# Kernel tuning notes

Measured on AMD Instinct MI355X. Metric: run time of the kernel, lower is better.

## Reference

```python
import jax, jax.numpy as jnp
import numpy as np

B, S, D = 2, 2048, 2048
H = 16
I = 8192  # intermediate_size
HD = I // H  # per-head intermediate dim = 512


def setup_inputs() -> dict:
    key = jax.random.key(0)
    ks = jax.random.split(key, 7)
    scale_d = 1.0 / np.sqrt(D)
    scale_i = 1.0 / np.sqrt(I)
    return {
        "x": jax.random.normal(ks[0], (B, S, D), dtype=jnp.float32),
        "adjacency": jax.random.uniform(ks[1], (B, H, S, S), dtype=jnp.float32) * (1.0 / S),
        "Wg": jax.random.normal(ks[2], (D, I), dtype=jnp.float32) * scale_d,
        "Wu": jax.random.normal(ks[3], (D, I), dtype=jnp.float32) * scale_d,
        "Wd": jax.random.normal(ks[4], (I, D), dtype=jnp.float32) * scale_i,
        "eps": jnp.zeros((H,), dtype=jnp.float32),
        "alpha": jnp.ones((H,), dtype=jnp.float32),
    }


def reference(x, adjacency, Wg, Wu, Wd, eps, alpha):
    # gate/up projections + SwiGLU: (B,S,I)
    gate = jnp.einsum("bsd,di->bsi", x, Wg)
    up = jnp.einsum("bsd,di->bsi", x, Wu)
    h_inter = jax.nn.silu(gate) * up
    # split into heads: (B,H,S,HD)
    h_heads = h_inter.reshape(B, S, H, HD).transpose(0, 2, 1, 3)
    # batched per-head GIN: (1+eps_h)*h + alpha_h * A_h @ h, all heads at once
    agg = jnp.einsum("bhst,bhtd->bhsd", adjacency, h_heads)
    e = (1.0 + eps)[None, :, None, None]
    a = alpha[None, :, None, None]
    h_gin = e * h_heads + a * agg
    # recombine heads -> (B,S,I), then down projection
    h_comb = h_gin.transpose(0, 2, 1, 3).reshape(B, S, I)
    return jnp.einsum("bsi,id->bsd", h_comb, Wd)
```

## Files before the change

### kernel.cpp

```cpp
#include <hip/hip_runtime.h>
#include <hip/hip_bf16.h>


typedef __bf16 bf16x8 __attribute__((ext_vector_type(8)));
typedef float f32x4 __attribute__((ext_vector_type(4)));

__device__ __forceinline__ unsigned short f2bf(float f) {
    union { float f; unsigned int u; } x; x.f = f;
    unsigned int r = x.u + 0x7fffu + ((x.u >> 16) & 1u);
    return (unsigned short)(r >> 16);
}
__device__ __forceinline__ float bf2f(unsigned short b) {
    union { unsigned int u; float f; } x; x.u = ((unsigned int)b) << 16;
    return x.f;
}

__device__ __forceinline__ void gload_lds16(const void* g, void* l) {
    __builtin_amdgcn_global_load_lds((const __attribute__((address_space(1))) void*)g,
                                     (__attribute__((address_space(3))) void*)l,
                                     16, 0, 0);
}

__device__ __forceinline__ void stage(unsigned short* lds, const unsigned short* g,
                                      int ld, int wave, int lane) {
    int rsub = lane >> 3;
    int j    = lane & 7;
    int jsw  = (j ^ rsub) << 3;
    const unsigned short* src = g + (size_t)(wave * 32 + rsub) * ld + jsw;
    unsigned short* dst = lds + (wave * 32) * 64;
#pragma unroll
    for (int c = 0; c < 4; ++c) {
        gload_lds16((const void*)(src + (size_t)c * 8 * ld), (void*)(dst + c * 8 * 64));
    }
}
__device__ __forceinline__ bf16x8 frag(const unsigned short* lds, int row, int k) {
    int byte = ((row * 64 + k) * 2) ^ ((row & 7) << 4);
    return *(const bf16x8*)((const char*)lds + byte);
}


__global__ void conv_kernel(const float* __restrict__ in, unsigned short* __restrict__ out) {
    size_t i = ((size_t)blockIdx.x * 256 + threadIdx.x) * 4;
    float4 v = *(const float4*)(in + i);
    ushort4 o; o.x = f2bf(v.x); o.y = f2bf(v.y); o.z = f2bf(v.z); o.w = f2bf(v.w);
    *(ushort4*)(out + i) = o;
}

__global__ void tconv_kernel(const float* __restrict__ in, unsigned short* __restrict__ out,
                             int R, int C) {
    __shared__ float tile[64][65];
    int nbc = C >> 6;
    int bc = blockIdx.x % nbc, br = blockIdx.x / nbc;
    int r0 = br * 64, c0 = bc * 64;
    int t = threadIdx.x;
#pragma unroll
    for (int i = 0; i < 4; ++i) {
        int idx = i * 256 + t;
        int r = idx >> 4, c4 = (idx & 15) * 4;
        float4 v = *(const float4*)(in + (size_t)(r0 + r) * C + c0 + c4);
        tile[r][c4] = v.x; tile[r][c4 + 1] = v.y; tile[r][c4 + 2] = v.z; tile[r][c4 + 3] = v.w;
    }
    __syncthreads();
#pragma unroll
    for (int i = 0; i < 4; ++i) {
        int idx = i * 256 + t;
        int c = idx >> 4, r4 = (idx & 15) * 4;
        ushort4 o;
        o.x = f2bf(tile[r4][c]); o.y = f2bf(tile[r4 + 1][c]);
        o.z = f2bf(tile[r4 + 2][c]); o.w = f2bf(tile[r4 + 3][c]);
        *(ushort4*)(out + (size_t)(c0 + c) * R + r0 + r4) = o;
    }
}

template<int EPI>
__global__ void __launch_bounds__(512, 2) gemm256(
    const unsigned short* __restrict__ Ag,
    const unsigned short* __restrict__ Bg,
    const unsigned short* __restrict__ gbuf_c,
    unsigned short* __restrict__ gbuf,
    unsigned short* __restrict__ hh,
    unsigned short* __restrict__ hhT)
{
    const int K = 2048;
    __shared__ unsigned short LDS[4][16384];
    int bid = (int)blockIdx.x;
    int lb = (bid & 7) * 64 + (bid >> 3);
    int nt = lb & 31, mt = lb >> 5;
    int tid = threadIdx.x, lane = tid & 63, wave = tid >> 6;
    int wm = wave >> 2, wn = wave & 3;
    int l15 = lane & 15, l4 = lane >> 4;

    f32x4 acc[8][4] = {};

    int jl = (lane & 7) ^ (lane >> 3);
    int prow0 = wave * 16 + (lane >> 3);
    int row0 = prow0 + ((jl & 4) << 5);
    int cc = (jl & 3) << 3;
    const unsigned short* srcA0 = Ag + (size_t)(mt * 256 + row0) * K + cc;
    const unsigned short* srcA1 = srcA0 + (size_t)8 * K;
    const unsigned short* srcB0 = Bg + (size_t)(nt * 256 + row0) * K + cc;
    const unsigned short* srcB1 = srcB0 + (size_t)8 * K;

    int cA = l15 * 128 + (((l4 + wm * 4) ^ (l15 & 7)) << 4);
    int cB = ((wn & 1) * 64 + l15) * 128 + (((l4 + ((wn >> 1) << 2)) ^ (l15 & 7)) << 4);

#define STAGE_A(t_) do { char* d_ = (char*)&LDS[(t_) & 3][0] + wave * 2048;              \
        gload_lds16((const void*)(srcA0 + (size_t)(t_) * 32), (void*)d_);                \
        gload_lds16((const void*)(srcA1 + (size_t)(t_) * 32), (void*)(d_ + 1024)); } while (0)
#define STAGE_B(t_) do { char* d_ = (char*)&LDS[(t_) & 3][8192] + wave * 2048;           \
        gload_lds16((const void*)(srcB0 + (size_t)(t_) * 32), (void*)d_);                \
        gload_lds16((const void*)(srcB1 + (size_t)(t_) * 32), (void*)(d_ + 1024)); } while (0)

    STAGE_A(0); STAGE_B(0);
    STAGE_A(1); STAGE_B(1);

    for (int t = 0; t < 64; ++t) {
        asm volatile("s_waitcnt vmcnt(4)" ::: "memory");
        __builtin_amdgcn_s_barrier();
        const char* Abase = (const char*)&LDS[t & 3][0];
        const char* Bbase = Abase + 16384;
        bool more = (t + 2) < 64;
        if (more) STAGE_A(t + 2);
        bf16x8 bf[4], af[4];
#pragma unroll
        for (int ni = 0; ni < 4; ++ni) bf[ni] = *(const bf16x8*)(Bbase + cB + ni * 2048);
#pragma unroll
        for (int mi = 0; mi < 4; ++mi) af[mi] = *(const bf16x8*)(Abase + cA + mi * 2048);
        __builtin_amdgcn_s_setprio(1);
#pragma unroll
        for (int mi = 0; mi < 4; ++mi)
#pragma unroll
            for (int ni = 0; ni < 4; ++ni)
                acc[mi][ni] = __builtin_amdgcn_mfma_f32_16x16x32_bf16(af[mi], bf[ni], acc[mi][ni], 0, 0, 0);
        __builtin_amdgcn_s_setprio(0);
        if (more) STAGE_B(t + 2);
#pragma unroll
        for (int mi = 0; mi < 4; ++mi) af[mi] = *(const bf16x8*)(Abase + cA + 8192 + mi * 2048);
        __builtin_amdgcn_s_setprio(1);
#pragma unroll
        for (int mi = 0; mi < 4; ++mi)
#pragma unroll
            for (int ni = 0; ni < 4; ++ni)
                acc[4 + mi][ni] = __builtin_amdgcn_mfma_f32_16x16x32_bf16(af[mi], bf[ni], acc[4 + mi][ni], 0, 0, 0);
        __builtin_amdgcn_s_setprio(0);
    }
#undef STAGE_A
#undef STAGE_B

    if (EPI == 0) {
        ushort4* g4 = (ushort4*)gbuf;
        size_t base = ((size_t)lb * 32) * 512 + tid;
#pragma unroll
        for (int a = 0; a < 8; ++a)
#pragma unroll
            for (int ni = 0; ni < 4; ++ni) {
                f32x4 v = acc[a][ni];
                ushort4 o;
                o.x = f2bf(v[0]); o.y = f2bf(v[1]); o.z = f2bf(v[2]); o.w = f2bf(v[3]);
                g4[base + (size_t)(a * 4 + ni) * 512] = o;
            }
    } else {
        const ushort4* g4 = (const ushort4*)gbuf_c;
        size_t base = ((size_t)lb * 32) * 512 + tid;
        int rowb = mt * 256 + wm * 128 + l4 * 4;
        int colb = nt * 256 + wn * 64 + l15;
        int b = mt >> 3;
#pragma unroll
        for (int a = 0; a < 8; ++a)
#pragma unroll
            for (int ni = 0; ni < 4; ++ni) {
                ushort4 gq = g4[base + (size_t)(a * 4 + ni) * 512];
                int row = rowb + a * 16;
                int n = colb + ni * 16;
                ushort4 hv;
#pragma unroll
                for (int r = 0; r < 4; ++r) {
                    float gv = bf2f(((const unsigned short*)&gq)[r]);
                    float u = acc[a][ni][r];
                    float h = gv / (1.f + __expf(-gv)) * u;
                    unsigned short hb = f2bf(h);
                    ((unsigned short*)&hv)[r] = hb;
                    hh[(size_t)(row + r) * 8192 + n] = hb;
                }
                *(ushort4*)(hhT + ((size_t)b * 8192 + n) * 2048 + (row & 2047)) = hv;
            }
    }
}

__global__ void __launch_bounds__(512) gemm_agg2(
    const float* __restrict__ adj,
    const unsigned short* __restrict__ hhT,
    const unsigned short* __restrict__ hh,
    const float* __restrict__ eps, const float* __restrict__ alpha,
    unsigned short* __restrict__ hcomb)
{
    const int S = 2048, HD = 512, I = 8192;
    __shared__ unsigned short As[128 * 40];
    __shared__ unsigned short Bs[512 * 40];
    int bid = (int)blockIdx.x;
    int lb = (bid & 7) * 64 + (bid >> 3);
    int pair = lb >> 4;
    int mt = lb & 15;
    int b = pair >> 4, h = pair & 15;
    int tid = threadIdx.x;
    int lane = tid & 63;
    int wave = tid >> 6;
    int wm = wave >> 2, wn = wave & 3;
    f32x4 acc[4][8] = {};

    const float* Ab = adj + ((size_t)pair * S + (size_t)mt * 128) * S;
    const unsigned short* Bb = hhT + ((size_t)b * I + (size_t)h * HD) * (size_t)S;

    float4 pa0, pa1;
    int4 pb0, pb1, pb2, pb3;
    int a_row0 = tid >> 3, a_c = (tid & 7) << 2;
    int b_row0 = tid >> 2, b_ch = (tid & 3) << 3;

#define AGG_LOAD(K0)                                                              \
    do {                                                                          \
        pa0 = *(const float4*)(Ab + (size_t)a_row0 * S + (K0) + a_c);             \
        pa1 = *(const float4*)(Ab + (size_t)(a_row0 + 64) * S + (K0) + a_c);      \
        pb0 = *(const int4*)(Bb + (size_t)b_row0 * S + (K0) + b_ch);              \
        pb1 = *(const int4*)(Bb + (size_t)(b_row0 + 128) * S + (K0) + b_ch);      \
        pb2 = *(const int4*)(Bb + (size_t)(b_row0 + 256) * S + (K0) + b_ch);      \
        pb3 = *(const int4*)(Bb + (size_t)(b_row0 + 384) * S + (K0) + b_ch);      \
    } while (0)

#define AGG_WRITE()                                                               \
    do {                                                                          \
        ushort4 o0, o1;                                                           \
        o0.x = f2bf(pa0.x); o0.y = f2bf(pa0.y); o0.z = f2bf(pa0.z); o0.w = f2bf(pa0.w); \
        o1.x = f2bf(pa1.x); o1.y = f2bf(pa1.y); o1.z = f2bf(pa1.z); o1.w = f2bf(pa1.w); \
        *(ushort4*)((char*)As + a_row0 * 80 + a_c * 2) = o0;                      \
        *(ushort4*)((char*)As + (a_row0 + 64) * 80 + a_c * 2) = o1;               \
        *(int4*)((char*)Bs + b_row0 * 80 + b_ch * 2) = pb0;                       \
        *(int4*)((char*)Bs + (b_row0 + 128) * 80 + b_ch * 2) = pb1;               \
        *(int4*)((char*)Bs + (b_row0 + 256) * 80 + b_ch * 2) = pb2;               \
        *(int4*)((char*)Bs + (b_row0 + 384) * 80 + b_ch * 2) = pb3;               \
    } while (0)

    AGG_LOAD(0);
    AGG_WRITE();
    __syncthreads();

    int lrow = lane & 15;
    int koff2 = ((lane >> 4) << 3) * 2;
    const char* aptr = (const char*)As + (wm * 64 + lrow) * 80 + koff2;
    const char* bptr = (const char*)Bs + (wn * 128 + lrow) * 80 + koff2;

    for (int step = 0; step < 64; ++step) {
        bool more = (step + 1) < 64;
        if (more) AGG_LOAD((step + 1) * 32);
        bf16x8 af[4], bfv[8];
#pragma unroll
        for (int mi = 0; mi < 4; ++mi) af[mi] = *(const bf16x8*)(aptr + mi * 16 * 80);
#pragma unroll
        for (int ni = 0; ni < 8; ++ni) bfv[ni] = *(const bf16x8*)(bptr + ni * 16 * 80);
#pragma unroll
        for (int mi = 0; mi < 4; ++mi)
#pragma unroll
            for (int ni = 0; ni < 8; ++ni)
                acc[mi][ni] = __builtin_amdgcn_mfma_f32_16x16x32_bf16(af[mi], bfv[ni], acc[mi][ni], 0, 0, 0);
        __syncthreads();
        if (more) {
            AGG_WRITE();
            __syncthreads();
        }
    }
#undef AGG_LOAD
#undef AGG_WRITE

    float e1 = 1.f + eps[h];
    float a1 = alpha[h];
    int s_base = mt * 128 + wm * 64;
    int d_base = wn * 128;
#pragma unroll
    for (int mi = 0; mi < 4; ++mi)
#pragma unroll
        for (int ni = 0; ni < 8; ++ni) {
            int sb = s_base + mi * 16 + ((lane >> 4) << 2);
            int d = d_base + ni * 16 + (lane & 15);
#pragma unroll
            for (int r = 0; r < 4; ++r) {
                size_t off = ((size_t)(b * S + sb + r)) * I + (size_t)h * HD + d;
                float hv = bf2f(hh[off]);
                hcomb[off] = f2bf(e1 * hv + a1 * acc[mi][ni][r]);
            }
        }
}

__global__ void __launch_bounds__(256) gemm_out(
    const unsigned short* __restrict__ hcomb,
    const unsigned short* __restrict__ WdT,
    float* __restrict__ out)
{
    const int K = 8192, N = 2048;
    __shared__ unsigned short As[128 * 64], Bs[128 * 64];
    int bid = blockIdx.x;
    int nt = bid & 15, mt = bid >> 4;
    int tid = threadIdx.x, wave = tid >> 6, lane = tid & 63;
    int wm = wave >> 1, wn = wave & 1;
    f32x4 acc[4][4] = {};
    const unsigned short* Ab = hcomb + (size_t)(mt * 128) * K;
    const unsigned short* Bb = WdT + (size_t)(nt * 128) * K;
    for (int k0 = 0; k0 < K; k0 += 64) {
        stage(As, Ab + k0, K, wave, lane);
        stage(Bs, Bb + k0, K, wave, lane);
        __syncthreads();
#pragma unroll
        for (int ki = 0; ki < 2; ++ki) {
            int kk = ki * 32 + ((lane >> 4) << 3);
            bf16x8 af[4], bfv[4];
#pragma unroll
            for (int mi = 0; mi < 4; ++mi) af[mi] = frag(As, wm * 64 + mi * 16 + (lane & 15), kk);
#pragma unroll
            for (int ni = 0; ni < 4; ++ni) bfv[ni] = frag(Bs, wn * 64 + ni * 16 + (lane & 15), kk);
#pragma unroll
            for (int mi = 0; mi < 4; ++mi)
#pragma unroll
                for (int ni = 0; ni < 4; ++ni)
                    acc[mi][ni] = __builtin_amdgcn_mfma_f32_16x16x32_bf16(af[mi], bfv[ni], acc[mi][ni], 0, 0, 0);
        }
        __syncthreads();
    }
    int m_off = mt * 128 + wm * 64, n_off = nt * 128 + wn * 64;
#pragma unroll
    for (int mi = 0; mi < 4; ++mi)
#pragma unroll
        for (int ni = 0; ni < 4; ++ni) {
            int mbase = m_off + mi * 16 + ((lane >> 4) << 2);
            int n = n_off + ni * 16 + (lane & 15);
#pragma unroll
            for (int r = 0; r < 4; ++r)
                out[(size_t)(mbase + r) * N + n] = acc[mi][ni][r];
        }
}

extern "C" void kernel_launch(void* const* d_in, const int* in_sizes, int n_in,
                              void* d_out, int out_size, void* d_ws, size_t ws_size,
                              hipStream_t stream) {
    const float* x     = (const float*)d_in[0];
    const float* adj   = (const float*)d_in[1];
    const float* Wg    = (const float*)d_in[2];
    const float* Wu    = (const float*)d_in[3];
    const float* Wd    = (const float*)d_in[4];
    const float* eps   = (const float*)d_in[5];
    const float* alpha = (const float*)d_in[6];
    float* out = (float*)d_out;

    unsigned short* ws    = (unsigned short*)d_ws;
    unsigned short* xb    = ws;
    unsigned short* WgT   = xb + (size_t)4096 * 2048;
    unsigned short* WuT   = WgT + (size_t)8192 * 2048;
    unsigned short* WdT   = WuT + (size_t)8192 * 2048;
    unsigned short* hh    = WdT + (size_t)2048 * 8192;
    unsigned short* hhT   = hh + (size_t)4096 * 8192;
    unsigned short* hcomb = hhT + (size_t)16384 * 2048;
    unsigned short* gbuf  = hcomb;

    conv_kernel<<<8192, 256, 0, stream>>>(x, xb);
    tconv_kernel<<<4096, 256, 0, stream>>>(Wg, WgT, 2048, 8192);
    tconv_kernel<<<4096, 256, 0, stream>>>(Wu, WuT, 2048, 8192);
    tconv_kernel<<<4096, 256, 0, stream>>>(Wd, WdT, 8192, 2048);
    gemm256<0><<<512, 512, 0, stream>>>(xb, WgT, nullptr, gbuf, nullptr, nullptr);
    gemm256<1><<<512, 512, 0, stream>>>(xb, WuT, gbuf, nullptr, hh, hhT);
    gemm_agg2<<<512, 512, 0, stream>>>(adj, hhT, hh, eps, alpha, hcomb);
    gemm_out<<<32 * 16, 256, 0, stream>>>(hcomb, WdT, out);
}
```

Baseline: 826.9 us.

## Double-buffer aggregation GEMM and pipeline down-projection with async LDS loads

```diff
diff --git a/kernel.cpp b/kernel.cpp
--- a/kernel.cpp
+++ b/kernel.cpp
@@ -19,23 +19,6 @@
     __builtin_amdgcn_global_load_lds((const __attribute__((address_space(1))) void*)g,
                                      (__attribute__((address_space(3))) void*)l,
                                      16, 0, 0);
-}
-
-__device__ __forceinline__ void stage(unsigned short* lds, const unsigned short* g,
-                                      int ld, int wave, int lane) {
-    int rsub = lane >> 3;
-    int j    = lane & 7;
-    int jsw  = (j ^ rsub) << 3;
-    const unsigned short* src = g + (size_t)(wave * 32 + rsub) * ld + jsw;
-    unsigned short* dst = lds + (wave * 32) * 64;
-#pragma unroll
-    for (int c = 0; c < 4; ++c) {
-        gload_lds16((const void*)(src + (size_t)c * 8 * ld), (void*)(dst + c * 8 * 64));
-    }
-}
-__device__ __forceinline__ bf16x8 frag(const unsigned short* lds, int row, int k) {
-    int byte = ((row * 64 + k) * 2) ^ ((row & 7) << 4);
-    return *(const bf16x8*)((const char*)lds + byte);
 }
 
 
@@ -115,7 +98,8 @@
     STAGE_A(1); STAGE_B(1);
 
     for (int t = 0; t < 64; ++t) {
-        asm volatile("s_waitcnt vmcnt(4)" ::: "memory");
+        if (t + 2 < 64) asm volatile("s_waitcnt vmcnt(4)" ::: "memory");
+        else            asm volatile("s_waitcnt vmcnt(0)" ::: "memory");
         __builtin_amdgcn_s_barrier();
         const char* Abase = (const char*)&LDS[t & 3][0];
         const char* Bbase = Abase + 16384;
@@ -187,7 +171,7 @@
     }
 }
 
-__global__ void __launch_bounds__(512) gemm_agg2(
+__global__ void __launch_bounds__(512, 2) gemm_agg3(
     const float* __restrict__ adj,
     const unsigned short* __restrict__ hhT,
     const unsigned short* __restrict__ hh,
@@ -195,8 +179,8 @@
     unsigned short* __restrict__ hcomb)
 {
     const int S = 2048, HD = 512, I = 8192;
-    __shared__ unsigned short As[128 * 40];
-    __shared__ unsigned short Bs[512 * 40];
+    __shared__ unsigned short As[2][128 * 40];
+    __shared__ unsigned short Bs[2][512 * 40];
     int bid = (int)blockIdx.x;
     int lb = (bid & 7) * 64 + (bid >> 3);
     int pair = lb >> 4;
@@ -211,64 +195,84 @@
     const float* Ab = adj + ((size_t)pair * S + (size_t)mt * 128) * S;
     const unsigned short* Bb = hhT + ((size_t)b * I + (size_t)h * HD) * (size_t)S;
 
-    float4 pa0, pa1;
-    int4 pb0, pb1, pb2, pb3;
     int a_row0 = tid >> 3, a_c = (tid & 7) << 2;
     int b_row0 = tid >> 2, b_ch = (tid & 3) << 3;
 
-#define AGG_LOAD(K0)                                                              \
-    do {                                                                          \
-        pa0 = *(const float4*)(Ab + (size_t)a_row0 * S + (K0) + a_c);             \
-        pa1 = *(const float4*)(Ab + (size_t)(a_row0 + 64) * S + (K0) + a_c);      \
-        pb0 = *(const int4*)(Bb + (size_t)b_row0 * S + (K0) + b_ch);              \
-        pb1 = *(const int4*)(Bb + (size_t)(b_row0 + 128) * S + (K0) + b_ch);      \
-        pb2 = *(const int4*)(Bb + (size_t)(b_row0 + 256) * S + (K0) + b_ch);      \
-        pb3 = *(const int4*)(Bb + (size_t)(b_row0 + 384) * S + (K0) + b_ch);      \
+    float4 pa0_0, pa1_0, pa0_1, pa1_1;
+    int4 pb0_0, pb1_0, pb2_0, pb3_0, pb0_1, pb1_1, pb2_1, pb3_1;
+
+#define AGG_LOAD(SET, K0)                                                               \
+    do {                                                                                \
+        pa0_##SET = *(const float4*)(Ab + (size_t)a_row0 * S + (K0) + a_c);             \
+        pa1_##SET = *(const float4*)(Ab + (size_t)(a_row0 + 64) * S + (K0) + a_c);      \
+        pb0_##SET = *(const int4*)(Bb + (size_t)b_row0 * S + (K0) + b_ch);              \
+        pb1_##SET = *(const int4*)(Bb + (size_t)(b_row0 + 128) * S + (K0) + b_ch);      \
+        pb2_##SET = *(const int4*)(Bb + (size_t)(b_row0 + 256) * S + (K0) + b_ch);      \
+        pb3_##SET = *(const int4*)(Bb + (size_t)(b_row0 + 384) * S + (K0) + b_ch);      \
     } while (0)
 
-#define AGG_WRITE()                                                               \
-    do {                                                                          \
-        ushort4 o0, o1;                                                           \
-        o0.x = f2bf(pa0.x); o0.y = f2bf(pa0.y); o0.z = f2bf(pa0.z); o0.w = f2bf(pa0.w); \
-        o1.x = f2bf(pa1.x); o1.y = f2bf(pa1.y); o1.z = f2bf(pa1.z); o1.w = f2bf(pa1.w); \
-        *(ushort4*)((char*)As + a_row0 * 80 + a_c * 2) = o0;                      \
-        *(ushort4*)((char*)As + (a_row0 + 64) * 80 + a_c * 2) = o1;               \
-        *(int4*)((char*)Bs + b_row0 * 80 + b_ch * 2) = pb0;                       \
-        *(int4*)((char*)Bs + (b_row0 + 128) * 80 + b_ch * 2) = pb1;               \
-        *(int4*)((char*)Bs + (b_row0 + 256) * 80 + b_ch * 2) = pb2;               \
-        *(int4*)((char*)Bs + (b_row0 + 384) * 80 + b_ch * 2) = pb3;               \
+#define AGG_WRITE(SET, BUF)                                                             \
+    do {                                                                                \
+        ushort4 o0, o1;                                                                 \
+        o0.x = f2bf(pa0_##SET.x); o0.y = f2bf(pa0_##SET.y);                             \
+        o0.z = f2bf(pa0_##SET.z); o0.w = f2bf(pa0_##SET.w);                             \
+        o1.x = f2bf(pa1_##SET.x); o1.y = f2bf(pa1_##SET.y);                             \
+        o1.z = f2bf(pa1_##SET.z); o1.w = f2bf(pa1_##SET.w);                             \
+        *(ushort4*)((char*)As[BUF] + a_row0 * 80 + a_c * 2) = o0;                       \
+        *(ushort4*)((char*)As[BUF] + (a_row0 + 64) * 80 + a_c * 2) = o1;                \
+        *(int4*)((char*)Bs[BUF] + b_row0 * 80 + b_ch * 2) = pb0_##SET;                  \
+        *(int4*)((char*)Bs[BUF] + (b_row0 + 128) * 80 + b_ch * 2) = pb1_##SET;          \
+        *(int4*)((char*)Bs[BUF] + (b_row0 + 256) * 80 + b_ch * 2) = pb2_##SET;          \
+        *(int4*)((char*)Bs[BUF] + (b_row0 + 384) * 80 + b_ch * 2) = pb3_##SET;          \
     } while (0)
-
-    AGG_LOAD(0);
-    AGG_WRITE();
-    __syncthreads();
 
     int lrow = lane & 15;
     int koff2 = ((lane >> 4) << 3) * 2;
-    const char* aptr = (const char*)As + (wm * 64 + lrow) * 80 + koff2;
-    const char* bptr = (const char*)Bs + (wn * 128 + lrow) * 80 + koff2;
-
-    for (int step = 0; step < 64; ++step) {
-        bool more = (step + 1) < 64;
-        if (more) AGG_LOAD((step + 1) * 32);
-        bf16x8 af[4], bfv[8];
-#pragma unroll
-        for (int mi = 0; mi < 4; ++mi) af[mi] = *(const bf16x8*)(aptr + mi * 16 * 80);
-#pragma unroll
-        for (int ni = 0; ni < 8; ++ni) bfv[ni] = *(const bf16x8*)(bptr + ni * 16 * 80);
-#pragma unroll
-        for (int mi = 0; mi < 4; ++mi)
-#pragma unroll
-            for (int ni = 0; ni < 8; ++ni)
-                acc[mi][ni] = __builtin_amdgcn_mfma_f32_16x16x32_bf16(af[mi], bfv[ni], acc[mi][ni], 0, 0, 0);
-        __syncthreads();
-        if (more) {
-            AGG_WRITE();
-            __syncthreads();
+    const char* aptr0 = (const char*)As[0] + (wm * 64 + lrow) * 80 + koff2;
+    const char* bptr0 = (const char*)Bs[0] + (wn * 128 + lrow) * 80 + koff2;
+    const char* aptr1 = (const char*)As[1] + (wm * 64 + lrow) * 80 + koff2;
+    const char* bptr1 = (const char*)Bs[1] + (wn * 128 + lrow) * 80 + koff2;
+
+#define AGG_COMPUTE(APTR, BPTR)                                                         \
+    do {                                                                                \
+        bf16x8 af[4], bfv[8];                                                           \
+        _Pragma("unroll")                                                               \
+        for (int mi = 0; mi < 4; ++mi) af[mi] = *(const bf16x8*)((APTR) + mi * 16 * 80);\
+        _Pragma("unroll")                                                               \
+        for (int ni = 0; ni < 8; ++ni) bfv[ni] = *(const bf16x8*)((BPTR) + ni * 16 * 80);\
+        __builtin_amdgcn_s_setprio(1);                                                  \
+        _Pragma("unroll")                                                               \
+        for (int mi = 0; mi < 4; ++mi)                                                  \
+            _Pragma("unroll")                                                           \
+            for (int ni = 0; ni < 8; ++ni)                                              \
+                acc[mi][ni] = __builtin_amdgcn_mfma_f32_16x16x32_bf16(af[mi], bfv[ni],  \
+                                                                      acc[mi][ni], 0, 0, 0); \
+        __builtin_amdgcn_s_setprio(0);                                                  \
+    } while (0)
+
+    AGG_LOAD(0, 0);
+    AGG_WRITE(0, 0);
+    AGG_LOAD(1, 32);
+    asm volatile("s_waitcnt lgkmcnt(0)" ::: "memory");
+    __builtin_amdgcn_s_barrier();
+
+    for (int s = 0; s < 64; s += 2) {
+        if (s + 2 < 64) AGG_LOAD(0, (s + 2) * 32);
+        AGG_COMPUTE(aptr0, bptr0);
+        AGG_WRITE(1, 1);
+        asm volatile("s_waitcnt lgkmcnt(0)" ::: "memory");
+        __builtin_amdgcn_s_barrier();
+        if (s + 3 < 64) AGG_LOAD(1, (s + 3) * 32);
+        AGG_COMPUTE(aptr1, bptr1);
+        if (s + 2 < 64) {
+            AGG_WRITE(0, 0);
+            asm volatile("s_waitcnt lgkmcnt(0)" ::: "memory");
+            __builtin_amdgcn_s_barrier();
         }
     }
 #undef AGG_LOAD
 #undef AGG_WRITE
+#undef AGG_COMPUTE
 
     float e1 = 1.f + eps[h];
     float a1 = alpha[h];
@@ -289,50 +293,79 @@
         }
 }
 
-__global__ void __launch_bounds__(256) gemm_out(
+__global__ void __launch_bounds__(512, 2) gemm_out2(
     const unsigned short* __restrict__ hcomb,
     const unsigned short* __restrict__ WdT,
     float* __restrict__ out)
 {
-    const int K = 8192, N = 2048;
-    __shared__ unsigned short As[128 * 64], Bs[128 * 64];
-    int bid = blockIdx.x;
-    int nt = bid & 15, mt = bid >> 4;
-    int tid = threadIdx.x, wave = tid >> 6, lane = tid & 63;
+    const int K = 8192;
+    __shared__ unsigned short LDS[4][12288];
+    int bid = (int)blockIdx.x;
+    int lb = (bid & 7) * 32 + (bid >> 3);
+    int mt = lb >> 4, nt = lb & 15;
+    int tid = threadIdx.x, lane = tid & 63, wave = tid >> 6;
     int wm = wave >> 1, wn = wave & 1;
+    int l15 = lane & 15, l4 = lane >> 4;
     f32x4 acc[4][4] = {};
-    const unsigned short* Ab = hcomb + (size_t)(mt * 128) * K;
-    const unsigned short* Bb = WdT + (size_t)(nt * 128) * K;
-    for (int k0 = 0; k0 < K; k0 += 64) {
-        stage(As, Ab + k0, K, wave, lane);
-        stage(Bs, Bb + k0, K, wave, lane);
-        __syncthreads();
-#pragma unroll
-        for (int ki = 0; ki < 2; ++ki) {
-            int kk = ki * 32 + ((lane >> 4) << 3);
-            bf16x8 af[4], bfv[4];
-#pragma unroll
-            for (int mi = 0; mi < 4; ++mi) af[mi] = frag(As, wm * 64 + mi * 16 + (lane & 15), kk);
-#pragma unroll
-            for (int ni = 0; ni < 4; ++ni) bfv[ni] = frag(Bs, wn * 64 + ni * 16 + (lane & 15), kk);
-#pragma unroll
-            for (int mi = 0; mi < 4; ++mi)
-#pragma unroll
-                for (int ni = 0; ni < 4; ++ni)
-                    acc[mi][ni] = __builtin_amdgcn_mfma_f32_16x16x32_bf16(af[mi], bfv[ni], acc[mi][ni], 0, 0, 0);
-        }
-        __syncthreads();
-    }
-    int m_off = mt * 128 + wm * 64, n_off = nt * 128 + wn * 64;
+
+    int jl = (lane & 7) ^ (lane >> 3);
+    int prowA = wave * 16 + (lane >> 3);
+    int rowA0 = prowA + ((jl & 4) << 5);
+    int ccA = (jl & 3) << 3;
+    const unsigned short* srcA0 = hcomb + (size_t)(mt * 256 + rowA0) * K + ccA;
+    const unsigned short* srcA1 = srcA0 + (size_t)8 * K;
+    int prowB = tid >> 3;
+    int jbl = (tid & 7) ^ (prowB & 7);
+    int rowB0 = prowB + ((jbl & 4) << 4);
+    int ccB = (jbl & 3) << 3;
+    const unsigned short* srcB0 = WdT + (size_t)(nt * 128 + rowB0) * K + ccB;
+
+    int cA0 = ((wm & 1) * 64 + l15) * 128 + (((((wm >> 1) << 2) + l4) ^ (l15 & 7)) << 4);
+    int cB0 = l15 * 128 + ((((wn << 2) + l4) ^ (l15 & 7)) << 4);
+
+#define OSTAGE(t_) do {                                                                  \
+        char* dA = (char*)&LDS[(t_) & 3][0] + wave * 2048;                               \
+        gload_lds16((const void*)(srcA0 + (size_t)(t_) * 32), (void*)dA);                \
+        gload_lds16((const void*)(srcA1 + (size_t)(t_) * 32), (void*)(dA + 1024));       \
+        char* dB = (char*)&LDS[(t_) & 3][8192] + wave * 1024;                            \
+        gload_lds16((const void*)(srcB0 + (size_t)(t_) * 32), (void*)dB);                \
+    } while (0)
+
+    OSTAGE(0); OSTAGE(1);
+
+    for (int t = 0; t < 256; ++t) {
+        if (t + 2 < 256) asm volatile("s_waitcnt vmcnt(3)" ::: "memory");
+        else             asm volatile("s_waitcnt vmcnt(0)" ::: "memory");
+        __builtin_amdgcn_s_barrier();
+        const char* Abase = (const char*)&LDS[t & 3][0];
+        const char* Bbase = Abase + 16384;
+        bool more = (t + 2) < 256;
+        bf16x8 af[4], bf[4];
+#pragma unroll
+        for (int ni = 0; ni < 4; ++ni) bf[ni] = *(const bf16x8*)(Bbase + cB0 + ni * 2048);
+        if (more) OSTAGE(t + 2);
+#pragma unroll
+        for (int mi = 0; mi < 4; ++mi) af[mi] = *(const bf16x8*)(Abase + cA0 + mi * 2048);
+        __builtin_amdgcn_s_setprio(1);
+#pragma unroll
+        for (int mi = 0; mi < 4; ++mi)
+#pragma unroll
+            for (int ni = 0; ni < 4; ++ni)
+                acc[mi][ni] = __builtin_amdgcn_mfma_f32_16x16x32_bf16(af[mi], bf[ni], acc[mi][ni], 0, 0, 0);
+        __builtin_amdgcn_s_setprio(0);
+    }
+#undef OSTAGE
+
+    int m_off = mt * 256 + wm * 64, n_off = nt * 128 + wn * 64;
 #pragma unroll
     for (int mi = 0; mi < 4; ++mi)
 #pragma unroll
         for (int ni = 0; ni < 4; ++ni) {
-            int mbase = m_off + mi * 16 + ((lane >> 4) << 2);
-            int n = n_off + ni * 16 + (lane & 15);
+            int mbase = m_off + mi * 16 + l4 * 4;
+            int n = n_off + ni * 16 + l15;
 #pragma unroll
             for (int r = 0; r < 4; ++r)
-                out[(size_t)(mbase + r) * N + n] = acc[mi][ni][r];
+                out[(size_t)(mbase + r) * 2048 + n] = acc[mi][ni][r];
         }
 }
 
@@ -364,6 +397,6 @@
     tconv_kernel<<<4096, 256, 0, stream>>>(Wd, WdT, 8192, 2048);
     gemm256<0><<<512, 512, 0, stream>>>(xb, WgT, nullptr, gbuf, nullptr, nullptr);
     gemm256<1><<<512, 512, 0, stream>>>(xb, WuT, gbuf, nullptr, hh, hhT);
-    gemm_agg2<<<512, 512, 0, stream>>>(adj, hhT, hh, eps, alpha, hcomb);
-    gemm_out<<<32 * 16, 256, 0, stream>>>(hcomb, WdT, out);
-}
+    gemm_agg3<<<512, 512, 0, stream>>>(adj, hhT, hh, eps, alpha, hcomb);
+    gemm_out2<<<256, 512, 0, stream>>>(hcomb, WdT, out);
+}
```

After: 762.7 us. 1.08x faster.
